# Kernel optimization log

Measured on AMD Instinct MI355X. Metric: run time of the kernel, lower is better.

The kernel has to match this reference:

```python
import jax, jax.numpy as jnp
import numpy as np

B, N, A, H = 500000, 256, 64, 100  # batch, num_nodes, num_adj (edges at node), hidden width


def setup_inputs() -> dict:
    key = jax.random.key(0)
    ks = jax.random.split(key, 12)
    data = jax.random.normal(ks[0], (B, N), dtype=jnp.float32)
    weights = jax.random.normal(ks[1], (A,), dtype=jnp.float32)
    # edge buffers (constants registered in the torch module)
    data_idx = jax.random.randint(ks[2], (A,), 0, N)
    edge_directions = 2 * jax.random.randint(ks[3], (A,), 0, 2) - 1  # values in {-1, +1}
    weight_idx = jnp.arange(A)
    # MLP params: Linear(A,H), Linear(H,H), Linear(H,H), Linear(H,1) (torch default-ish init scale)
    def lin(k, fan_in, fan_out):
        s = 1.0 / np.sqrt(fan_in)
        kw, kb = jax.random.split(k)
        W = jax.random.uniform(kw, (fan_in, fan_out), jnp.float32, -s, s)
        b = jax.random.uniform(kb, (fan_out,), jnp.float32, -s, s)
        return W, b
    W1, b1 = lin(ks[4], A, H)
    W2, b2 = lin(ks[5], H, H)
    W3, b3 = lin(ks[6], H, H)
    W4, b4 = lin(ks[7], H, 1)
    return dict(data=data, weights=weights, W1=W1, b1=b1, W2=W2, b2=b2,
                W3=W3, b3=b3, W4=W4, b4=b4, data_idx=data_idx,
                edge_directions=edge_directions, weight_idx=weight_idx)


def reference(data, weights, W1, b1, W2, b2, W3, b3, W4, b4,
              data_idx, edge_directions, weight_idx):
    # per-edge gate: relu(weight * direction), shape [A]
    gate = jax.nn.relu(weights[weight_idx] * edge_directions.astype(weights.dtype))
    # fused gather over node columns + elementwise gate: [B, A]
    x = data[:, data_idx] * gate
    # stacked MLP: A -> H -> H -> H -> 1 with ReLU
    x = jax.nn.relu(x @ W1 + b1)
    x = jax.nn.relu(x @ W2 + b2)
    x = jax.nn.relu(x @ W3 + b3)
    return x @ W4 + b4  # [B, 1]
```

## Files before the change

### kernel.cpp

```cpp
#include <hip/hip_runtime.h>

#define BB 500000
#define NN 256
#define AA 64
#define HH 100

typedef short short8 __attribute__((ext_vector_type(8)));
typedef float float4v __attribute__((ext_vector_type(4)));

#define MFMA16(a, b, c) __builtin_amdgcn_mfma_f32_16x16x32_bf16((a), (b), (c), 0, 0, 0)

__device__ __forceinline__ short f2bf(float f) {
    unsigned u = __builtin_bit_cast(unsigned, f);
    u = (u + 0x7fffu + ((u >> 16) & 1u)) >> 16;
    return (short)u;
}

#define OFF_W1T   0
#define OFF_W2T   16128
#define OFF_W3T   46592
#define OFF_B1    77056
#define OFF_B2    77504
#define OFF_B3    77952
#define OFF_GATE  78400
#define OFF_X     78656
#define LDS_TOTAL 148288

#define ROWS_PER_TILE 256
#define NTILES ((BB + ROWS_PER_TILE - 1) / ROWS_PER_TILE)

__global__ void __launch_bounds__(512, 2)
nodal_mlp(const float* __restrict__ data, const float* __restrict__ weights,
          const float* __restrict__ W1, const float* __restrict__ b1,
          const float* __restrict__ W2, const float* __restrict__ b2,
          const float* __restrict__ W3, const float* __restrict__ b3,
          const float* __restrict__ W4, const float* __restrict__ b4,
          const int* __restrict__ didx, const int* __restrict__ edir,
          const int* __restrict__ widx, float* __restrict__ out)
{
    extern __shared__ char smem[];
    short* w1T  = (short*)(smem + OFF_W1T);
    short* w2T  = (short*)(smem + OFF_W2T);
    short* w3T  = (short*)(smem + OFF_W3T);
    float* b1p  = (float*)(smem + OFF_B1);
    float* b2p  = (float*)(smem + OFF_B2);
    float* b3p  = (float*)(smem + OFF_B3);
    float* gate = (float*)(smem + OFF_GATE);

    const int tid  = threadIdx.x;
    const int wave = tid >> 6;
    const int lane = tid & 63;
    const int m    = lane & 15;
    const int quad = lane >> 4;

    short* Xw = (short*)(smem + OFF_X) + wave * (32 * 136);

    if (tid < AA)
        gate[tid] = fmaxf(weights[widx[tid]] * (float)edir[tid], 0.f);
    if (tid < 112) {
        b1p[tid] = (tid < HH) ? b1[tid] : 0.f;
        b2p[tid] = (tid < HH) ? b2[tid] : 0.f;
        b3p[tid] = (tid < HH) ? b3[tid] : 0.f;
    }
    for (int i = tid; i < 112 * 72; i += 512) w1T[i] = 0;
    for (int i = tid; i < 112 * 136; i += 512) { w2T[i] = 0; w3T[i] = 0; }
    for (int i = lane; i < 32 * 16; i += 64) {
        int r = i >> 4, k = 112 + (i & 15);
        Xw[r * 136 + k] = 0;
    }
    __syncthreads();
    for (int j = tid; j < AA * HH; j += 512) {
        int k = j / HH, n = j - k * HH;
        w1T[n * 72 + k] = f2bf(gate[k] * W1[j]);
    }
    for (int j = tid; j < HH * HH; j += 512) {
        int k = j / HH, n = j - k * HH;
        w2T[n * 136 + k] = f2bf(W2[j]);
        w3T[n * 136 + k] = f2bf(W3[j]);
    }
    __syncthreads();

    short8 w4f[4];
    #pragma unroll
    for (int ks = 0; ks < 4; ++ks) {
        #pragma unroll
        for (int j = 0; j < 8; ++j) {
            int k = ks * 32 + quad * 8 + j;
            w4f[ks][j] = (m == 0 && k < HH) ? f2bf(W4[k]) : (short)0;
        }
    }
    const float b4v   = b4[0];
    const int  colOff = didx[lane];

    float pf[32];
    int t = (int)blockIdx.x;
    {
        int r0 = t * ROWS_PER_TILE + wave * 32;
        const float* p = data + (size_t)colOff;
        if (r0 + 32 <= BB) {
            const float* q = p + (size_t)r0 * NN;
            #pragma unroll
            for (int r = 0; r < 32; ++r) pf[r] = q[r * NN];
        } else {
            #pragma unroll
            for (int r = 0; r < 32; ++r) {
                int row = r0 + r; row = row < BB ? row : BB - 1;
                pf[r] = p[(size_t)row * NN];
            }
        }
    }

    for (; t < NTILES; t += gridDim.x) {
        const int r0 = t * ROWS_PER_TILE + wave * 32;

        #pragma unroll
        for (int r = 0; r < 32; ++r)
            Xw[r * 136 + lane] = f2bf(pf[r]);

        {
            int tn = t + (int)gridDim.x;
            if (tn < NTILES) {
                int r0n = tn * ROWS_PER_TILE + wave * 32;
                const float* p = data + (size_t)colOff;
                if (r0n + 32 <= BB) {
                    const float* q = p + (size_t)r0n * NN;
                    #pragma unroll
                    for (int r = 0; r < 32; ++r) pf[r] = q[r * NN];
                } else {
                    #pragma unroll
                    for (int r = 0; r < 32; ++r) {
                        int row = r0n + r; row = row < BB ? row : BB - 1;
                        pf[r] = p[(size_t)row * NN];
                    }
                }
            }
        }

        {
            short8 a1[2][2];
            #pragma unroll
            for (int sub = 0; sub < 2; ++sub)
                #pragma unroll
                for (int ks = 0; ks < 2; ++ks)
                    a1[sub][ks] = *(const short8*)(Xw + (sub * 16 + m) * 136 + ks * 32 + quad * 8);
            #pragma unroll
            for (int nt = 0; nt < 7; ++nt) {
                const short* wp = w1T + (nt * 16 + m) * 72 + quad * 8;
                short8 w0 = *(const short8*)(wp);
                short8 w1v = *(const short8*)(wp + 32);
                float bias = b1p[nt * 16 + m];
                #pragma unroll
                for (int sub = 0; sub < 2; ++sub) {
                    float4v c = {0.f, 0.f, 0.f, 0.f};
                    c = MFMA16(a1[sub][0], w0, c);
                    c = MFMA16(a1[sub][1], w1v, c);
                    #pragma unroll
                    for (int i = 0; i < 4; ++i)
                        Xw[(sub * 16 + quad * 4 + i) * 136 + nt * 16 + m] =
                            f2bf(fmaxf(c[i] + bias, 0.f));
                }
            }
        }

        #pragma unroll
        for (int L = 0; L < 2; ++L) {
            const short* wT = L ? w3T : w2T;
            const float* bp = L ? b3p : b2p;
            short8 a[2][4];
            #pragma unroll
            for (int sub = 0; sub < 2; ++sub)
                #pragma unroll
                for (int ks = 0; ks < 4; ++ks)
                    a[sub][ks] = *(const short8*)(Xw + (sub * 16 + m) * 136 + ks * 32 + quad * 8);
            #pragma unroll
            for (int nt = 0; nt < 7; ++nt) {
                const short* wp = wT + (nt * 16 + m) * 136 + quad * 8;
                short8 wf[4];
                #pragma unroll
                for (int ks = 0; ks < 4; ++ks)
                    wf[ks] = *(const short8*)(wp + ks * 32);
                float bias = bp[nt * 16 + m];
                #pragma unroll
                for (int sub = 0; sub < 2; ++sub) {
                    float4v c = {0.f, 0.f, 0.f, 0.f};
                    #pragma unroll
                    for (int ks = 0; ks < 4; ++ks)
                        c = MFMA16(a[sub][ks], wf[ks], c);
                    #pragma unroll
                    for (int i = 0; i < 4; ++i)
                        Xw[(sub * 16 + quad * 4 + i) * 136 + nt * 16 + m] =
                            f2bf(fmaxf(c[i] + bias, 0.f));
                }
            }
        }

        #pragma unroll
        for (int sub = 0; sub < 2; ++sub) {
            float4v c = {0.f, 0.f, 0.f, 0.f};
            #pragma unroll
            for (int ks = 0; ks < 4; ++ks) {
                short8 a = *(const short8*)(Xw + (sub * 16 + m) * 136 + ks * 32 + quad * 8);
                c = MFMA16(a, w4f[ks], c);
            }
            if (m == 0) {
                #pragma unroll
                for (int i = 0; i < 4; ++i) {
                    int row = r0 + sub * 16 + quad * 4 + i;
                    if (row < BB) out[row] = c[i] + b4v;
                }
            }
        }
    }
}

extern "C" void kernel_launch(void* const* d_in, const int* in_sizes, int n_in,
                              void* d_out, int out_size, void* d_ws, size_t ws_size,
                              hipStream_t stream) {
    (void)in_sizes; (void)n_in; (void)d_ws; (void)ws_size; (void)out_size;
    const float* data    = (const float*)d_in[0];
    const float* weights = (const float*)d_in[1];
    const float* W1      = (const float*)d_in[2];
    const float* b1      = (const float*)d_in[3];
    const float* W2      = (const float*)d_in[4];
    const float* b2      = (const float*)d_in[5];
    const float* W3      = (const float*)d_in[6];
    const float* b3      = (const float*)d_in[7];
    const float* W4      = (const float*)d_in[8];
    const float* b4      = (const float*)d_in[9];
    const int*   didx    = (const int*)d_in[10];
    const int*   edir    = (const int*)d_in[11];
    const int*   widx    = (const int*)d_in[12];
    float* out = (float*)d_out;

    hipFuncSetAttribute((const void*)nodal_mlp,
                        hipFuncAttributeMaxDynamicSharedMemorySize, LDS_TOTAL);
    nodal_mlp<<<256, 512, LDS_TOTAL, stream>>>(
        data, weights, W1, b1, W2, b2, W3, b3, W4, b4, didx, edir, widx, out);
}
```

Baseline: 697.0 us.

## Load full rows with coalesced float4 reads and gather columns via ds_bpermute

Per-lane scattered scalar loads of the gathered columns are replaced with fully coalesced float4 loads of whole 256-float rows. The 64 selected columns are then picked out in registers with cross-lane ds_bpermute plus selects. Loads are split into 8-row groups double-buffered against the gather, and the next tile's first group is prefetched. The aim is to cut per-request gather overhead and improve memory efficiency, at the cost of reading every row in full, four bpermutes per element, and shorter prefetch distance.

```diff
diff --git a/kernel.cpp b/kernel.cpp
--- a/kernel.cpp
+++ b/kernel.cpp
@@ -7,11 +7,16 @@
 
 typedef short short8 __attribute__((ext_vector_type(8)));
 typedef float float4v __attribute__((ext_vector_type(4)));
+typedef int   int4v   __attribute__((ext_vector_type(4)));
 
 #define MFMA16(a, b, c) __builtin_amdgcn_mfma_f32_16x16x32_bf16((a), (b), (c), 0, 0, 0)
 
 __device__ __forceinline__ short f2bf(float f) {
     unsigned u = __builtin_bit_cast(unsigned, f);
+    u = (u + 0x7fffu + ((u >> 16) & 1u)) >> 16;
+    return (short)u;
+}
+__device__ __forceinline__ short u2bf(unsigned u) {
     u = (u + 0x7fffu + ((u >> 16) & 1u)) >> 16;
     return (short)u;
 }
@@ -28,6 +33,39 @@
 
 #define ROWS_PER_TILE 256
 #define NTILES ((BB + ROWS_PER_TILE - 1) / ROWS_PER_TILE)
+
+#define LOAD_GROUP(dst, tile, g)                                            \
+    {                                                                       \
+        int r0_ = (tile) * ROWS_PER_TILE + wave * 32 + (g) * 8;             \
+        if (r0_ + 8 <= BB) {                                                \
+            const float* q_ = data + (size_t)r0_ * NN + lane * 4;           \
+            _Pragma("unroll")                                               \
+            for (int r_ = 0; r_ < 8; ++r_)                                  \
+                dst[r_] = *(const float4v*)(q_ + (size_t)r_ * NN);          \
+        } else {                                                            \
+            _Pragma("unroll")                                               \
+            for (int r_ = 0; r_ < 8; ++r_) {                                \
+                int row_ = r0_ + r_; row_ = row_ < BB ? row_ : BB - 1;      \
+                dst[r_] = *(const float4v*)(data + (size_t)row_ * NN + lane * 4); \
+            }                                                               \
+        }                                                                   \
+    }
+
+#define GATHER_GROUP(src, g)                                                \
+    {                                                                       \
+        _Pragma("unroll")                                                   \
+        for (int r_ = 0; r_ < 8; ++r_) {                                    \
+            int4v iv_ = __builtin_bit_cast(int4v, src[r_]);                 \
+            int g0_ = __builtin_amdgcn_ds_bpermute(baddr, iv_[0]);          \
+            int g1_ = __builtin_amdgcn_ds_bpermute(baddr, iv_[1]);          \
+            int g2_ = __builtin_amdgcn_ds_bpermute(baddr, iv_[2]);          \
+            int g3_ = __builtin_amdgcn_ds_bpermute(baddr, iv_[3]);          \
+            int lo_ = c0 ? g1_ : g0_;                                       \
+            int hi_ = c0 ? g3_ : g2_;                                       \
+            unsigned u_ = (unsigned)(c1 ? hi_ : lo_);                       \
+            Xw[((g) * 8 + r_) * 136 + lane] = u2bf(u_);                     \
+        }                                                                   \
+    }
 
 __global__ void __launch_bounds__(512, 2)
 nodal_mlp(const float* __restrict__ data, const float* __restrict__ weights,
@@ -89,52 +127,31 @@
             w4f[ks][j] = (m == 0 && k < HH) ? f2bf(W4[k]) : (short)0;
         }
     }
-    const float b4v   = b4[0];
-    const int  colOff = didx[lane];
-
-    float pf[32];
+    const float b4v = b4[0];
+
+    const int  cidx  = didx[lane];
+    const int  baddr = (cidx >> 2) << 2;
+    const bool c0    = (cidx & 1) != 0;
+    const bool c1    = (cidx & 2) != 0;
+
+    float4v bufA[8], bufB[8];
     int t = (int)blockIdx.x;
-    {
-        int r0 = t * ROWS_PER_TILE + wave * 32;
-        const float* p = data + (size_t)colOff;
-        if (r0 + 32 <= BB) {
-            const float* q = p + (size_t)r0 * NN;
-            #pragma unroll
-            for (int r = 0; r < 32; ++r) pf[r] = q[r * NN];
-        } else {
-            #pragma unroll
-            for (int r = 0; r < 32; ++r) {
-                int row = r0 + r; row = row < BB ? row : BB - 1;
-                pf[r] = p[(size_t)row * NN];
-            }
-        }
-    }
+    LOAD_GROUP(bufA, t, 0);
 
     for (; t < NTILES; t += gridDim.x) {
         const int r0 = t * ROWS_PER_TILE + wave * 32;
 
-        #pragma unroll
-        for (int r = 0; r < 32; ++r)
-            Xw[r * 136 + lane] = f2bf(pf[r]);
-
+        LOAD_GROUP(bufB, t, 1);
+        GATHER_GROUP(bufA, 0);
+        LOAD_GROUP(bufA, t, 2);
+        GATHER_GROUP(bufB, 1);
+        LOAD_GROUP(bufB, t, 3);
+        GATHER_GROUP(bufA, 2);
         {
             int tn = t + (int)gridDim.x;
-            if (tn < NTILES) {
-                int r0n = tn * ROWS_PER_TILE + wave * 32;
-                const float* p = data + (size_t)colOff;
-                if (r0n + 32 <= BB) {
-                    const float* q = p + (size_t)r0n * NN;
-                    #pragma unroll
-                    for (int r = 0; r < 32; ++r) pf[r] = q[r * NN];
-                } else {
-                    #pragma unroll
-                    for (int r = 0; r < 32; ++r) {
-                        int row = r0n + r; row = row < BB ? row : BB - 1;
-                        pf[r] = p[(size_t)row * NN];
-                    }
-                }
-            }
-        }
+            if (tn < NTILES) LOAD_GROUP(bufA, tn, 0);
+        }
+        GATHER_GROUP(bufB, 3);
 
         {
             short8 a1[2][2];
```

After: 695.8 us. About the same (-0.2%).
